# Kernel optimization log

Hardware: AMD Instinct MI355X
Metric: run time of the kernel (lower is better)

Reference implementation:

```python
import jax, jax.numpy as jnp
import numpy as np

STATE_LEN = 128
SEQ_LEN = 2048
NUM_ITERS = 2
DIM_IN = 1024
DIM_H = 64
BATCH = 2
T_TOTAL = SEQ_LEN + 2 * STATE_LEN  # 2304
NEG = -1e30  # large-negative causal mask (avoids -inf NaNs under autodiff)


def _ln(x, g, b):
    m = jnp.mean(x, axis=-1, keepdims=True)
    v = jnp.var(x, axis=-1, keepdims=True)
    return (x - m) / jnp.sqrt(v + 1e-5) * g + b


def setup_inputs() -> dict:
    key = jax.random.key(0)
    ks = jax.random.split(key, 16)

    def w(k, fi, fo):
        # torch nn.Linear-style fan-in scaled init (keeps logits O(1))
        return jax.random.normal(k, (fi, fo), jnp.float32) / np.sqrt(fi)

    return {
        "x": jax.random.normal(ks[0], (BATCH, T_TOTAL, DIM_IN), jnp.float32),
        "Wh": w(ks[1], DIM_IN, DIM_H),
        "Whs": w(ks[2], DIM_IN, DIM_H),
        "Whe": w(ks[3], DIM_IN, DIM_H),
        "Wk": w(ks[4], DIM_H, DIM_H),
        "Wq": w(ks[5], DIM_H, DIM_H),
        "Wv": w(ks[6], DIM_H, DIM_H),
        "Wks": w(ks[7], DIM_H, DIM_H),
        "Wqs": w(ks[8], DIM_H, DIM_H),
        "Wvs": w(ks[9], DIM_H, DIM_H),
        "Wke": w(ks[10], DIM_H, DIM_H),
        "Wqe": w(ks[11], DIM_H, DIM_H),
        "Wve": w(ks[12], DIM_H, DIM_H),
        "ln_g": jnp.ones((DIM_IN,), jnp.float32),
        "ln_b": jnp.zeros((DIM_IN,), jnp.float32),
        "ln_gs": jnp.ones((DIM_IN,), jnp.float32),
        "ln_bs": jnp.zeros((DIM_IN,), jnp.float32),
        "ln_ge": jnp.ones((DIM_IN,), jnp.float32),
        "ln_be": jnp.zeros((DIM_IN,), jnp.float32),
        "cope_emb": jax.random.normal(ks[13], (DIM_H, T_TOTAL), jnp.float32),
    }


def reference(x, Wh, Whs, Whe, Wk, Wq, Wv, Wks, Wqs, Wvs, Wke, Wqe, Wve,
              ln_g, ln_b, ln_gs, ln_bs, ln_ge, ln_be, cope_emb):
    S = STATE_LEN
    # extract_state: [state_start | seq | state_end] along token dim
    xs, xm, xe = x[:, :S], x[:, S:-S], x[:, -S:]
    xm = _ln(xm, ln_g, ln_b)
    xs = _ln(xs, ln_gs, ln_bs)
    xe = _ln(xe, ln_ge, ln_be)

    mem = xm @ Wh                 # (B, L, D)
    mem_s = xs @ Whs              # (B, S, D)
    mem_e = xe @ Whe              # (B, S, D)

    scale = 1.0 / np.sqrt(DIM_H)  # xformers default scale (beta=None)
    tril = jnp.tril(jnp.ones((T_TOTAL, T_TOTAL), bool))
    mask = jnp.where(tril, 0.0, NEG)  # log of lower-triangular ones

    mem_full = None
    for ix in range(NUM_ITERS):
        k = jnp.concatenate([mem_s @ Wks, mem @ Wk, mem_e @ Wke], axis=1)  # (B,T,D)
        q = jnp.concatenate([mem_s @ Wqs, mem @ Wq, mem_e @ Wqe], axis=1)
        v = jnp.concatenate([mem_s @ Wvs, mem @ Wv, mem_e @ Wve], axis=1)

        logits = jnp.einsum('btd,bsd->bts', q, k)  # unscaled, as in CoPE gates
        if ix == 0:
            # CoPE: sigmoid-gated reverse cumsum positions + interpolated embedding bias
            gates = jax.nn.sigmoid(logits)
            pos = jnp.flip(jnp.cumsum(jnp.flip(gates, -1), axis=-1), -1)
            pos = jnp.minimum(pos, float(T_TOTAL - 1))
            pos_floor = jnp.floor(pos)
            pos_ceil = jnp.ceil(pos)
            logits_int = jnp.einsum('btd,dn->btn', q, cope_emb)  # (B,T,T)
            lc = jnp.take_along_axis(logits_int, pos_ceil.astype(jnp.int32), axis=-1)
            lf = jnp.take_along_axis(logits_int, pos_floor.astype(jnp.int32), axis=-1)
            wfrac = pos - pos_floor
            bias = lc * wfrac + lf * (1.0 - wfrac)
            scores = logits * scale + mask + bias
        else:
            scores = logits * scale + mask

        attn = jax.nn.softmax(scores, axis=-1)
        mem_full = jnp.einsum('bts,bsd->btd', attn, v)  # (B,T,D)
        if ix < NUM_ITERS - 1:
            mem_s, mem, mem_e = mem_full[:, :S], mem_full[:, S:-S], mem_full[:, -S:]
    return mem_full
```

## Files before the change

### kernel.cpp

```cpp
#include <hip/hip_runtime.h>

#define T_TOT 2304
#define S_LEN 128
#define D_IN  1024
#define D_H   64
#define BATCH 2
#define NROW  (BATCH * T_TOT)
#define CH    (T_TOT / 256)
#define SCALE 0.125f
#define KCHUNKS 8
#define KCW   (D_IN / KCHUNKS)

typedef unsigned short u16;
typedef __attribute__((ext_vector_type(8))) short short8;
typedef __attribute__((ext_vector_type(4))) float f32x4;
typedef __attribute__((ext_vector_type(4))) unsigned short u16x4;

static __device__ __forceinline__ u16 f2bf(float f) {
    unsigned u = __float_as_uint(f);
    unsigned r = (u + 0x7fffu + ((u >> 16) & 1u)) >> 16;
    return (u16)r;
}
static __device__ __forceinline__ float bf2f(u16 s) {
    return __uint_as_float((unsigned)s << 16);
}

__global__ __launch_bounds__(256) void k_ln(
    const float* __restrict__ x,
    const float* __restrict__ ln_g,  const float* __restrict__ ln_b,
    const float* __restrict__ ln_gs, const float* __restrict__ ln_bs,
    const float* __restrict__ ln_ge, const float* __restrict__ ln_be,
    u16* __restrict__ xn_hi, u16* __restrict__ xn_lo)
{
    __shared__ float red1[256], red2[256];
    const int row = blockIdx.x;
    const int t = row % T_TOT;
    const int tid = threadIdx.x;

    const float *gg, *bb;
    if (t < S_LEN)               { gg = ln_gs; bb = ln_bs; }
    else if (t >= T_TOT - S_LEN) { gg = ln_ge; bb = ln_be; }
    else                         { gg = ln_g;  bb = ln_b;  }

    const float4 xv = *(const float4*)(x + (size_t)row * D_IN + 4 * tid);
    float s  = xv.x + xv.y + xv.z + xv.w;
    float s2 = xv.x * xv.x + xv.y * xv.y + xv.z * xv.z + xv.w * xv.w;
    red1[tid] = s; red2[tid] = s2; __syncthreads();
    for (int off = 128; off > 0; off >>= 1) {
        if (tid < off) { red1[tid] += red1[tid + off]; red2[tid] += red2[tid + off]; }
        __syncthreads();
    }
    const float mean = red1[0] * (1.f / D_IN);
    const float var  = red2[0] * (1.f / D_IN) - mean * mean;
    const float rstd = rsqrtf(var + 1e-5f);

    const float4 gv = *(const float4*)(gg + 4 * tid);
    const float4 bv = *(const float4*)(bb + 4 * tid);
    float o0 = (xv.x - mean) * rstd * gv.x + bv.x;
    float o1 = (xv.y - mean) * rstd * gv.y + bv.y;
    float o2 = (xv.z - mean) * rstd * gv.z + bv.z;
    float o3 = (xv.w - mean) * rstd * gv.w + bv.w;

    u16x4 hv, lv;
    hv[0] = f2bf(o0); lv[0] = f2bf(o0 - bf2f(hv[0]));
    hv[1] = f2bf(o1); lv[1] = f2bf(o1 - bf2f(hv[1]));
    hv[2] = f2bf(o2); lv[2] = f2bf(o2 - bf2f(hv[2]));
    hv[3] = f2bf(o3); lv[3] = f2bf(o3 - bf2f(hv[3]));
    *(u16x4*)(xn_hi + (size_t)row * D_IN + 4 * tid) = hv;
    *(u16x4*)(xn_lo + (size_t)row * D_IN + 4 * tid) = lv;
}

#define WPREP_N (3 * D_H * D_IN)
__global__ __launch_bounds__(256) void k_prep(
    const float* __restrict__ Wh, const float* __restrict__ Whs, const float* __restrict__ Whe,
    const float* __restrict__ cope,
    u16* __restrict__ wT_hi, u16* __restrict__ wT_lo,
    u16* __restrict__ cT_hi, u16* __restrict__ cT_lo)
{
    const int gid = blockIdx.x * 256 + threadIdx.x;
    if (gid < WPREP_N) {
        const int seg = gid >> 16;
        const int o = gid & 65535;
        const int j = o >> 10, k = o & 1023;
        const float* W = seg == 0 ? Wh : (seg == 1 ? Whs : Whe);
        const float f = W[k * D_H + j];
        const u16 hi = f2bf(f);
        wT_hi[gid] = hi;
        wT_lo[gid] = f2bf(f - bf2f(hi));
    } else {
        const int idx = gid - WPREP_N;
        if (idx < T_TOT * D_H) {
            const int n = idx >> 6, d = idx & 63;
            const float f = cope[(size_t)d * T_TOT + n];
            const u16 hi = f2bf(f);
            cT_hi[idx] = hi;
            cT_lo[idx] = f2bf(f - bf2f(hi));
        }
    }
}

__global__ __launch_bounds__(256) void k_hgemm(
    const u16* __restrict__ xn_hi, const u16* __restrict__ xn_lo,
    const u16* __restrict__ wT_hi, const u16* __restrict__ wT_lo,
    float* __restrict__ h_part)
{
    const int tile = blockIdx.x;
    const int kc   = blockIdx.y;
    const int k0   = kc * KCW;
    const int tt = tile % 36;
    const int seg = tt < 2 ? 1 : (tt >= 34 ? 2 : 0);

    __shared__ u16 Bh[64 * KCW];
    __shared__ u16 Bl[64 * KCW];

    const int tid = threadIdx.x;
    {
        const int r = tid >> 2;
        const int c0 = (tid & 3) * 32;
        const u16* sh = wT_hi + ((size_t)seg * D_H + r) * D_IN + k0 + c0;
        const u16* sl = wT_lo + ((size_t)seg * D_H + r) * D_IN + k0 + c0;
        const int sw = (r & 7) << 3;
        #pragma unroll
        for (int u = 0; u < 4; ++u) {
            const int col = c0 + 8 * u;
            *(short8*)&Bh[r * KCW + (col ^ sw)] = *(const short8*)(sh + 8 * u);
            *(short8*)&Bl[r * KCW + (col ^ sw)] = *(const short8*)(sl + 8 * u);
        }
    }
    __syncthreads();

    const int w = tid >> 6;
    const int lane = tid & 63;
    const int l15 = lane & 15, lg4 = lane >> 4;
    const int row0 = tile * 64 + w * 16;

    const size_t abase = (size_t)(row0 + l15) * D_IN + k0 + 8 * lg4;
    f32x4 acc[4] = {};

    #pragma unroll
    for (int kk = 0; kk < KCW / 32; ++kk) {
        short8 ah = *(const short8*)(xn_hi + abase + kk * 32);
        short8 al = *(const short8*)(xn_lo + abase + kk * 32);
        #pragma unroll
        for (int j = 0; j < 4; ++j) {
            const int brow = j * 16 + l15;
            const int col = (kk * 32 + 8 * lg4) ^ ((brow & 7) << 3);
            short8 bh = *(const short8*)&Bh[brow * KCW + col];
            short8 bl = *(const short8*)&Bl[brow * KCW + col];
            acc[j] = __builtin_amdgcn_mfma_f32_16x16x32_bf16(al, bh, acc[j], 0, 0, 0);
            acc[j] = __builtin_amdgcn_mfma_f32_16x16x32_bf16(ah, bl, acc[j], 0, 0, 0);
            acc[j] = __builtin_amdgcn_mfma_f32_16x16x32_bf16(ah, bh, acc[j], 0, 0, 0);
        }
    }
    float* hp = h_part + (size_t)kc * ((size_t)NROW * D_H);
    #pragma unroll
    for (int j = 0; j < 4; ++j)
        #pragma unroll
        for (int r = 0; r < 4; ++r)
            hp[(size_t)(row0 + 4 * lg4 + r) * D_H + j * 16 + l15] = acc[j][r];
}

__global__ __launch_bounds__(256) void k_hred(
    const float* __restrict__ h_part, float* __restrict__ h)
{
    const size_t idx = (size_t)blockIdx.x * 256 + threadIdx.x;
    const size_t N = (size_t)NROW * D_H;
    float s = 0.f;
    #pragma unroll
    for (int kc = 0; kc < KCHUNKS; ++kc) s += h_part[kc * N + idx];
    h[idx] = s;
}

template <bool SPLIT>
__global__ __launch_bounds__(192) void k_qkv(
    const float* __restrict__ hin,
    const float* __restrict__ Wk,  const float* __restrict__ Wq,  const float* __restrict__ Wv,
    const float* __restrict__ Wks, const float* __restrict__ Wqs, const float* __restrict__ Wvs,
    const float* __restrict__ Wke, const float* __restrict__ Wqe, const float* __restrict__ Wve,
    u16* __restrict__ q_hi, u16* __restrict__ q_lo,
    u16* __restrict__ k_hi, u16* __restrict__ k_lo,
    u16* __restrict__ vT)
{
    __shared__ float hr[D_H];
    const int bid = blockIdx.x;
    const int b = bid / T_TOT, t = bid % T_TOT;
    const int tid = threadIdx.x;

    const float* hrow = hin + ((size_t)b * T_TOT + t) * D_H;
    if (tid < D_H) hr[tid] = hrow[tid];
    __syncthreads();

    const int which = tid >> 6, j = tid & 63;
    const float* W;
    if (t < S_LEN)               W = which == 0 ? Wks : (which == 1 ? Wqs : Wvs);
    else if (t >= T_TOT - S_LEN) W = which == 0 ? Wke : (which == 1 ? Wqe : Wve);
    else                         W = which == 0 ? Wk  : (which == 1 ? Wq  : Wv);

    float acc = 0.f;
    #pragma unroll
    for (int d = 0; d < D_H; ++d) acc += hr[d] * W[d * D_H + j];

    const size_t idx = ((size_t)b * T_TOT + t) * D_H + j;
    u16 hi = f2bf(acc);
    if (which == 0) {
        k_hi[idx] = hi;
        if (SPLIT) k_lo[idx] = f2bf(acc - bf2f(hi));
    } else if (which == 1) {
        q_hi[idx] = hi;
        if (SPLIT) q_lo[idx] = f2bf(acc - bf2f(hi));
    } else {
        vT[((size_t)b * D_H + j) * T_TOT + t] = hi;
    }
}

__global__ __launch_bounds__(256) void k_score2(
    const u16* __restrict__ a_hi, const u16* __restrict__ a_lo,
    const u16* __restrict__ k_hi, const u16* __restrict__ k_lo,
    const u16* __restrict__ c_hi, const u16* __restrict__ c_lo,
    float* __restrict__ logits, float* __restrict__ lint)
{
    const int b  = blockIdx.z;
    const int s0 = blockIdx.x * 128;
    const int t0 = blockIdx.y * 64 + (threadIdx.x >> 6) * 16;
    const int lane = threadIdx.x & 63;
    const int l15 = lane & 15, lg4 = lane >> 4;

    const size_t a_off = ((size_t)(b * T_TOT + t0 + l15)) * D_H + 8 * lg4;
    const short8 ah0 = *(const short8*)(a_hi + a_off);
    const short8 ah1 = *(const short8*)(a_hi + a_off + 32);
    const short8 al0 = *(const short8*)(a_lo + a_off);
    const short8 al1 = *(const short8*)(a_lo + a_off + 32);

    const size_t orow_off = ((size_t)(b * T_TOT + t0 + 4 * lg4)) * T_TOT + s0 + l15;

    const u16* bh = k_hi + (size_t)b * (T_TOT * D_H);
    const u16* bl = k_lo + (size_t)b * (T_TOT * D_H);
    float* o = logits + orow_off;
    #pragma unroll
    for (int pass = 0; pass < 2; ++pass) {
        #pragma unroll
        for (int ni = 0; ni < 8; ++ni) {
            const size_t b_off = ((size_t)(s0 + ni * 16 + l15)) * D_H + 8 * lg4;
            short8 bh0 = *(const short8*)(bh + b_off);
            short8 bh1 = *(const short8*)(bh + b_off + 32);
            short8 bl0 = *(const short8*)(bl + b_off);
            short8 bl1 = *(const short8*)(bl + b_off + 32);
            f32x4 acc = {0.f, 0.f, 0.f, 0.f};
            acc = __builtin_amdgcn_mfma_f32_16x16x32_bf16(al0, bh0, acc, 0, 0, 0);
            acc = __builtin_amdgcn_mfma_f32_16x16x32_bf16(al1, bh1, acc, 0, 0, 0);
            acc = __builtin_amdgcn_mfma_f32_16x16x32_bf16(ah0, bl0, acc, 0, 0, 0);
            acc = __builtin_amdgcn_mfma_f32_16x16x32_bf16(ah1, bl1, acc, 0, 0, 0);
            acc = __builtin_amdgcn_mfma_f32_16x16x32_bf16(ah0, bh0, acc, 0, 0, 0);
            acc = __builtin_amdgcn_mfma_f32_16x16x32_bf16(ah1, bh1, acc, 0, 0, 0);
            #pragma unroll
            for (int r = 0; r < 4; ++r)
                o[(size_t)r * T_TOT + ni * 16] = acc[r];
        }
        bh = c_hi; bl = c_lo;
        o = lint + orow_off;
    }
}

__global__ __launch_bounds__(256) void k_score(
    const u16* __restrict__ a_hi, const u16* __restrict__ b_hi,
    float* __restrict__ out)
{
    const int b  = blockIdx.z;
    const int s0 = blockIdx.x * 128;
    if (s0 > blockIdx.y * 64 + 63) return;
    const int t0 = blockIdx.y * 64 + (threadIdx.x >> 6) * 16;
    const int lane = threadIdx.x & 63;
    const int l15 = lane & 15, lg4 = lane >> 4;

    const size_t a_off = ((size_t)(b * T_TOT + t0 + l15)) * D_H + 8 * lg4;
    short8 ah0 = *(const short8*)(a_hi + a_off);
    short8 ah1 = *(const short8*)(a_hi + a_off + 32);

    const u16* bh = b_hi + (size_t)b * (T_TOT * D_H);
    float* orow = out + ((size_t)(b * T_TOT + t0 + 4 * lg4)) * T_TOT + s0 + l15;

    #pragma unroll
    for (int ni = 0; ni < 8; ++ni) {
        const size_t b_off = ((size_t)(s0 + ni * 16 + l15)) * D_H + 8 * lg4;
        short8 bh0 = *(const short8*)(bh + b_off);
        short8 bh1 = *(const short8*)(bh + b_off + 32);
        f32x4 acc = {0.f, 0.f, 0.f, 0.f};
        acc = __builtin_amdgcn_mfma_f32_16x16x32_bf16(ah0, bh0, acc, 0, 0, 0);
        acc = __builtin_amdgcn_mfma_f32_16x16x32_bf16(ah1, bh1, acc, 0, 0, 0);
        #pragma unroll
        for (int r = 0; r < 4; ++r)
            orow[(size_t)r * T_TOT + ni * 16] = acc[r];
    }
}

__global__ __launch_bounds__(256) void k_pv(
    const float* __restrict__ pbuf, const u16* __restrict__ vT,
    float* __restrict__ out)
{
    const int b  = blockIdx.z;
    const int t0 = blockIdx.x * 16;
    const int j0 = (threadIdx.x >> 6) * 16;
    const int lane = threadIdx.x & 63;
    const int l15 = lane & 15, lg4 = lane >> 4;

    const u16* pb = (const u16*)pbuf
        + ((size_t)(b * T_TOT + t0 + l15)) * (2 * (size_t)T_TOT) + 8 * lg4;
    const u16* vb = vT + ((size_t)(b * D_H + j0 + l15)) * T_TOT + 8 * lg4;

    f32x4 a0 = {}, a1 = {}, a2 = {}, a3 = {};
    const int smax = t0 + 16;
    int sc = 0;
    for (; sc + 128 <= smax; sc += 128) {
        short8 p0 = *(const short8*)(pb + sc);
        short8 v0 = *(const short8*)(vb + sc);
        short8 p1 = *(const short8*)(pb + sc + 32);
        short8 v1 = *(const short8*)(vb + sc + 32);
        short8 p2 = *(const short8*)(pb + sc + 64);
        short8 v2 = *(const short8*)(vb + sc + 64);
        short8 p3 = *(const short8*)(pb + sc + 96);
        short8 v3 = *(const short8*)(vb + sc + 96);
        a0 = __builtin_amdgcn_mfma_f32_16x16x32_bf16(p0, v0, a0, 0, 0, 0);
        a1 = __builtin_amdgcn_mfma_f32_16x16x32_bf16(p1, v1, a1, 0, 0, 0);
        a2 = __builtin_amdgcn_mfma_f32_16x16x32_bf16(p2, v2, a2, 0, 0, 0);
        a3 = __builtin_amdgcn_mfma_f32_16x16x32_bf16(p3, v3, a3, 0, 0, 0);
    }
    for (; sc < smax; sc += 32) {
        short8 p0 = *(const short8*)(pb + sc);
        short8 v0 = *(const short8*)(vb + sc);
        a0 = __builtin_amdgcn_mfma_f32_16x16x32_bf16(p0, v0, a0, 0, 0, 0);
    }
    f32x4 acc = (a0 + a1) + (a2 + a3);
    float* obase = out + ((size_t)(b * T_TOT + t0 + 4 * lg4)) * D_H + j0 + l15;
    #pragma unroll
    for (int r = 0; r < 4; ++r) obase[(size_t)r * D_H] = acc[r];
}

template <bool COPE>
__global__ __launch_bounds__(256) void k_erow(
    const float* __restrict__ logits,
    const float* __restrict__ lint,
    float* __restrict__ pbase)
{
    __shared__ float lg[T_TOT];
    __shared__ float extra[COPE ? 2 * T_TOT : 2];
    __shared__ float wtot[4], wmax[4], wsum[4];

    const int row = blockIdx.x;
    const int t = row % T_TOT;
    const int tid = threadIdx.x;
    const int lane = tid & 63, wid = tid >> 6;
    const float* lrow = logits + (size_t)row * T_TOT;

    if (COPE) {
        for (int r = 0; r < CH; ++r) { int s = tid + 256 * r; lg[s] = lrow[s]; }
    } else {
        for (int r = 0; r < CH; ++r) { int s = tid + 256 * r; if (s <= t) lg[s] = lrow[s]; }
    }
    __syncthreads();

    if (COPE) {
        const int base = tid * CH;
        float gv[CH];
        float lsum = 0.f;
        #pragma unroll
        for (int u = 0; u < CH; ++u) {
            float g = 1.f / (1.f + expf(-lg[base + u]));
            gv[u] = g;
            lsum += g;
        }
        float cs = lsum;
        #pragma unroll
        for (int off = 1; off < 64; off <<= 1) {
            float n = __shfl_up(cs, off);
            if (lane >= off) cs += n;
        }
        if (lane == 63) wtot[wid] = cs;
        __syncthreads();
        float pre = 0.f, tot = 0.f;
        #pragma unroll
        for (int w = 0; w < 4; ++w) {
            float vv = wtot[w];
            tot += vv;
            if (w < wid) pre += vv;
        }
        float run = pre + cs - lsum;
        #pragma unroll
        for (int u = 0; u < CH; ++u) {
            float p = fminf(tot - run, (float)(T_TOT - 1));
            extra[base + u] = p;
            run += gv[u];
        }
        const float* lintrow = lint + (size_t)row * T_TOT;
        for (int r = 0; r < CH; ++r) { int s = tid + 256 * r; extra[T_TOT + s] = lintrow[s]; }
        __syncthreads();
    }

    float scv[CH];
    float mx = -3.4e38f;
    #pragma unroll
    for (int r = 0; r < CH; ++r) {
        int sidx = tid + 256 * r;
        float sc = -3.4e38f;
        if (sidx <= t) {
            sc = lg[sidx] * SCALE;
            if (COPE) {
                float p = extra[sidx];
                float pf = floorf(p);
                int fi = (int)pf;
                int ci = (int)ceilf(p);
                float w = p - pf;
                sc += extra[T_TOT + ci] * w + extra[T_TOT + fi] * (1.f - w);
            }
            mx = fmaxf(mx, sc);
        }
        scv[r] = sc;
    }
    #pragma unroll
    for (int off = 32; off > 0; off >>= 1) mx = fmaxf(mx, __shfl_xor(mx, off));
    if (lane == 0) wmax[wid] = mx;
    __syncthreads();
    mx = fmaxf(fmaxf(wmax[0], wmax[1]), fmaxf(wmax[2], wmax[3]));

    float pvv[CH];
    float psum = 0.f;
    #pragma unroll
    for (int r = 0; r < CH; ++r) {
        int sidx = tid + 256 * r;
        float pv = 0.f;
        if (sidx <= t) { pv = expf(scv[r] - mx); psum += pv; }
        pvv[r] = pv;
    }
    #pragma unroll
    for (int off = 32; off > 0; off >>= 1) psum += __shfl_xor(psum, off);
    if (lane == 0) wsum[wid] = psum;
    __syncthreads();
    const float inv = 1.f / (wsum[0] + wsum[1] + wsum[2] + wsum[3]);

    u16* prow = (u16*)(pbase + (size_t)row * T_TOT);
    #pragma unroll
    for (int r = 0; r < CH; ++r) {
        int sidx = tid + 256 * r;
        prow[sidx] = f2bf(pvv[r] * inv);
    }
}

extern "C" void kernel_launch(void* const* d_in, const int* in_sizes, int n_in,
                              void* d_out, int out_size, void* d_ws, size_t ws_size,
                              hipStream_t stream) {
    const float* x    = (const float*)d_in[0];
    const float* Wh   = (const float*)d_in[1];
    const float* Whs  = (const float*)d_in[2];
    const float* Whe  = (const float*)d_in[3];
    const float* Wk   = (const float*)d_in[4];
    const float* Wq   = (const float*)d_in[5];
    const float* Wv   = (const float*)d_in[6];
    const float* Wks  = (const float*)d_in[7];
    const float* Wqs  = (const float*)d_in[8];
    const float* Wvs  = (const float*)d_in[9];
    const float* Wke  = (const float*)d_in[10];
    const float* Wqe  = (const float*)d_in[11];
    const float* Wve  = (const float*)d_in[12];
    const float* ln_g  = (const float*)d_in[13];
    const float* ln_b  = (const float*)d_in[14];
    const float* ln_gs = (const float*)d_in[15];
    const float* ln_bs = (const float*)d_in[16];
    const float* ln_ge = (const float*)d_in[17];
    const float* ln_be = (const float*)d_in[18];
    const float* cope  = (const float*)d_in[19];

    float* out = (float*)d_out;

    const size_t N = (size_t)NROW * D_H;
    char* W = (char*)d_ws;
    u16* xn_hi  = (u16*)W;    W += (size_t)NROW * D_IN * 2;
    u16* xn_lo  = (u16*)W;    W += (size_t)NROW * D_IN * 2;
    u16* wT_hi  = (u16*)W;    W += (size_t)3 * D_H * D_IN * 2;
    u16* wT_lo  = (u16*)W;    W += (size_t)3 * D_H * D_IN * 2;
    float* h    = (float*)W;  W += N * 4;
    u16* q_hi   = (u16*)W;    W += N * 2;
    u16* q_lo   = (u16*)W;    W += N * 2;
    u16* k_hi   = (u16*)W;    W += N * 2;
    u16* k_lo   = (u16*)W;    W += N * 2;
    u16* vT     = (u16*)W;    W += N * 2;
    u16* cT_hi  = (u16*)W;    W += (size_t)T_TOT * D_H * 2;
    u16* cT_lo  = (u16*)W;    W += (size_t)T_TOT * D_H * 2;
    float* logits = (float*)W; W += (size_t)BATCH * T_TOT * T_TOT * 4;
    float* lint   = (float*)W; W += (size_t)BATCH * T_TOT * T_TOT * 4;
    float* mem1   = (float*)W;

    float* h_part = lint;

    const dim3 sg(T_TOT / 128, T_TOT / 64, BATCH);

    k_ln<<<NROW, 256, 0, stream>>>(x, ln_g, ln_b, ln_gs, ln_bs, ln_ge, ln_be,
                                   xn_hi, xn_lo);
    k_prep<<<(WPREP_N + T_TOT * D_H + 255) / 256, 256, 0, stream>>>(
        Wh, Whs, Whe, cope, wT_hi, wT_lo, cT_hi, cT_lo);
    k_hgemm<<<dim3(NROW / 64, KCHUNKS), 256, 0, stream>>>(xn_hi, xn_lo, wT_hi, wT_lo, h_part);
    k_hred<<<(int)(N / 256), 256, 0, stream>>>(h_part, h);

    k_qkv<true><<<NROW, 192, 0, stream>>>(h, Wk, Wq, Wv, Wks, Wqs, Wvs, Wke, Wqe, Wve,
                                          q_hi, q_lo, k_hi, k_lo, vT);
    k_score2<<<sg, 256, 0, stream>>>(q_hi, q_lo, k_hi, k_lo, cT_hi, cT_lo, logits, lint);
    k_erow<true><<<NROW, 256, 0, stream>>>(logits, lint, lint);
    k_pv<<<dim3(T_TOT / 16, 1, BATCH), 256, 0, stream>>>(lint, vT, mem1);

    k_qkv<false><<<NROW, 192, 0, stream>>>(mem1, Wk, Wq, Wv, Wks, Wqs, Wvs, Wke, Wqe, Wve,
                                           q_hi, q_lo, k_hi, k_lo, vT);
    k_score<<<sg, 256, 0, stream>>>(q_hi, k_hi, logits);
    k_erow<false><<<NROW, 256, 0, stream>>>(logits, nullptr, lint);
    k_pv<<<dim3(T_TOT / 16, 1, BATCH), 256, 0, stream>>>(lint, vT, out);
}
```

Before: 189.4 us.

## Fuse second attention iteration into split-K flash attention and split PV

Replaces the second iteration's score, softmax-row and PV kernels with a flash-attention kernel that computes scores, online softmax and PV per 16-row tile across key chunks, followed by a merge kernel. This removes the full T×T logits write and read for the second pass. The first-pass PV is also split over key chunks with a reduction kernel to balance the causal triangle, and the first score kernel uses 64-wide column tiles for more blocks. It adds extra partial buffers and merge launches, and uses bf16 P with online rescaling.

```diff
diff --git a/kernel.cpp b/kernel.cpp
--- a/kernel.cpp
+++ b/kernel.cpp
@@ -10,6 +10,10 @@
 #define SCALE 0.125f
 #define KCHUNKS 8
 #define KCW   (D_IN / KCHUNKS)
+#define TB    16
+#define FCH   288
+#define NSC   8
+#define NTBLK (T_TOT / TB)
 
 typedef unsigned short u16;
 typedef __attribute__((ext_vector_type(8))) short short8;
@@ -220,8 +224,9 @@
     float* __restrict__ logits, float* __restrict__ lint)
 {
     const int b  = blockIdx.z;
-    const int s0 = blockIdx.x * 128;
-    const int t0 = blockIdx.y * 64 + (threadIdx.x >> 6) * 16;
+    const int s0 = blockIdx.x * 64;
+    const int wid = threadIdx.x >> 6;
+    const int t0 = blockIdx.y * 64 + wid * 16;
     const int lane = threadIdx.x & 63;
     const int l15 = lane & 15, lg4 = lane >> 4;
 
@@ -236,10 +241,11 @@
     const u16* bh = k_hi + (size_t)b * (T_TOT * D_H);
     const u16* bl = k_lo + (size_t)b * (T_TOT * D_H);
     float* o = logits + orow_off;
+
     #pragma unroll
     for (int pass = 0; pass < 2; ++pass) {
         #pragma unroll
-        for (int ni = 0; ni < 8; ++ni) {
+        for (int ni = 0; ni < 4; ++ni) {
             const size_t b_off = ((size_t)(s0 + ni * 16 + l15)) * D_H + 8 * lg4;
             short8 bh0 = *(const short8*)(bh + b_off);
             short8 bh1 = *(const short8*)(bh + b_off + 32);
@@ -261,88 +267,13 @@
     }
 }
 
-__global__ __launch_bounds__(256) void k_score(
-    const u16* __restrict__ a_hi, const u16* __restrict__ b_hi,
-    float* __restrict__ out)
-{
-    const int b  = blockIdx.z;
-    const int s0 = blockIdx.x * 128;
-    if (s0 > blockIdx.y * 64 + 63) return;
-    const int t0 = blockIdx.y * 64 + (threadIdx.x >> 6) * 16;
-    const int lane = threadIdx.x & 63;
-    const int l15 = lane & 15, lg4 = lane >> 4;
-
-    const size_t a_off = ((size_t)(b * T_TOT + t0 + l15)) * D_H + 8 * lg4;
-    short8 ah0 = *(const short8*)(a_hi + a_off);
-    short8 ah1 = *(const short8*)(a_hi + a_off + 32);
-
-    const u16* bh = b_hi + (size_t)b * (T_TOT * D_H);
-    float* orow = out + ((size_t)(b * T_TOT + t0 + 4 * lg4)) * T_TOT + s0 + l15;
-
-    #pragma unroll
-    for (int ni = 0; ni < 8; ++ni) {
-        const size_t b_off = ((size_t)(s0 + ni * 16 + l15)) * D_H + 8 * lg4;
-        short8 bh0 = *(const short8*)(bh + b_off);
-        short8 bh1 = *(const short8*)(bh + b_off + 32);
-        f32x4 acc = {0.f, 0.f, 0.f, 0.f};
-        acc = __builtin_amdgcn_mfma_f32_16x16x32_bf16(ah0, bh0, acc, 0, 0, 0);
-        acc = __builtin_amdgcn_mfma_f32_16x16x32_bf16(ah1, bh1, acc, 0, 0, 0);
-        #pragma unroll
-        for (int r = 0; r < 4; ++r)
-            orow[(size_t)r * T_TOT + ni * 16] = acc[r];
-    }
-}
-
-__global__ __launch_bounds__(256) void k_pv(
-    const float* __restrict__ pbuf, const u16* __restrict__ vT,
-    float* __restrict__ out)
-{
-    const int b  = blockIdx.z;
-    const int t0 = blockIdx.x * 16;
-    const int j0 = (threadIdx.x >> 6) * 16;
-    const int lane = threadIdx.x & 63;
-    const int l15 = lane & 15, lg4 = lane >> 4;
-
-    const u16* pb = (const u16*)pbuf
-        + ((size_t)(b * T_TOT + t0 + l15)) * (2 * (size_t)T_TOT) + 8 * lg4;
-    const u16* vb = vT + ((size_t)(b * D_H + j0 + l15)) * T_TOT + 8 * lg4;
-
-    f32x4 a0 = {}, a1 = {}, a2 = {}, a3 = {};
-    const int smax = t0 + 16;
-    int sc = 0;
-    for (; sc + 128 <= smax; sc += 128) {
-        short8 p0 = *(const short8*)(pb + sc);
-        short8 v0 = *(const short8*)(vb + sc);
-        short8 p1 = *(const short8*)(pb + sc + 32);
-        short8 v1 = *(const short8*)(vb + sc + 32);
-        short8 p2 = *(const short8*)(pb + sc + 64);
-        short8 v2 = *(const short8*)(vb + sc + 64);
-        short8 p3 = *(const short8*)(pb + sc + 96);
-        short8 v3 = *(const short8*)(vb + sc + 96);
-        a0 = __builtin_amdgcn_mfma_f32_16x16x32_bf16(p0, v0, a0, 0, 0, 0);
-        a1 = __builtin_amdgcn_mfma_f32_16x16x32_bf16(p1, v1, a1, 0, 0, 0);
-        a2 = __builtin_amdgcn_mfma_f32_16x16x32_bf16(p2, v2, a2, 0, 0, 0);
-        a3 = __builtin_amdgcn_mfma_f32_16x16x32_bf16(p3, v3, a3, 0, 0, 0);
-    }
-    for (; sc < smax; sc += 32) {
-        short8 p0 = *(const short8*)(pb + sc);
-        short8 v0 = *(const short8*)(vb + sc);
-        a0 = __builtin_amdgcn_mfma_f32_16x16x32_bf16(p0, v0, a0, 0, 0, 0);
-    }
-    f32x4 acc = (a0 + a1) + (a2 + a3);
-    float* obase = out + ((size_t)(b * T_TOT + t0 + 4 * lg4)) * D_H + j0 + l15;
-    #pragma unroll
-    for (int r = 0; r < 4; ++r) obase[(size_t)r * D_H] = acc[r];
-}
-
-template <bool COPE>
 __global__ __launch_bounds__(256) void k_erow(
     const float* __restrict__ logits,
     const float* __restrict__ lint,
     float* __restrict__ pbase)
 {
     __shared__ float lg[T_TOT];
-    __shared__ float extra[COPE ? 2 * T_TOT : 2];
+    __shared__ float extra[2 * T_TOT];
     __shared__ float wtot[4], wmax[4], wsum[4];
 
     const int row = blockIdx.x;
@@ -351,14 +282,10 @@
     const int lane = tid & 63, wid = tid >> 6;
     const float* lrow = logits + (size_t)row * T_TOT;
 
-    if (COPE) {
-        for (int r = 0; r < CH; ++r) { int s = tid + 256 * r; lg[s] = lrow[s]; }
-    } else {
-        for (int r = 0; r < CH; ++r) { int s = tid + 256 * r; if (s <= t) lg[s] = lrow[s]; }
-    }
+    for (int r = 0; r < CH; ++r) { int s = tid + 256 * r; lg[s] = lrow[s]; }
     __syncthreads();
 
-    if (COPE) {
+    {
         const int base = tid * CH;
         float gv[CH];
         float lsum = 0.f;
@@ -403,14 +330,12 @@
         float sc = -3.4e38f;
         if (sidx <= t) {
             sc = lg[sidx] * SCALE;
-            if (COPE) {
-                float p = extra[sidx];
-                float pf = floorf(p);
-                int fi = (int)pf;
-                int ci = (int)ceilf(p);
-                float w = p - pf;
-                sc += extra[T_TOT + ci] * w + extra[T_TOT + fi] * (1.f - w);
-            }
+            float p = extra[sidx];
+            float pf = floorf(p);
+            int fi = (int)pf;
+            int ci = (int)ceilf(p);
+            float w = p - pf;
+            sc += extra[T_TOT + ci] * w + extra[T_TOT + fi] * (1.f - w);
             mx = fmaxf(mx, sc);
         }
         scv[r] = sc;
@@ -442,6 +367,205 @@
         int sidx = tid + 256 * r;
         prow[sidx] = f2bf(pvv[r] * inv);
     }
+}
+
+__global__ __launch_bounds__(256) void k_pv(
+    const float* __restrict__ pbuf, const u16* __restrict__ vT,
+    float* __restrict__ opart)
+{
+    const int b  = blockIdx.z;
+    const int scn = blockIdx.y;
+    const int bx = blockIdx.x;
+    const int t0 = bx * 16;
+    const int sstart = scn * FCH;
+    const int send = min(sstart + FCH, t0 + 16);
+    if (sstart >= send) return;
+
+    const int j0 = (threadIdx.x >> 6) * 16;
+    const int lane = threadIdx.x & 63;
+    const int l15 = lane & 15, lg4 = lane >> 4;
+
+    const u16* pb = (const u16*)pbuf
+        + ((size_t)(b * T_TOT + t0 + l15)) * (2 * (size_t)T_TOT) + 8 * lg4;
+    const u16* vb = vT + ((size_t)(b * D_H + j0 + l15)) * T_TOT + 8 * lg4;
+
+    f32x4 a0 = {}, a1 = {}, a2 = {}, a3 = {};
+    int s = sstart;
+    for (; s + 128 <= send; s += 128) {
+        short8 p0 = *(const short8*)(pb + s);
+        short8 v0 = *(const short8*)(vb + s);
+        short8 p1 = *(const short8*)(pb + s + 32);
+        short8 v1 = *(const short8*)(vb + s + 32);
+        short8 p2 = *(const short8*)(pb + s + 64);
+        short8 v2 = *(const short8*)(vb + s + 64);
+        short8 p3 = *(const short8*)(pb + s + 96);
+        short8 v3 = *(const short8*)(vb + s + 96);
+        a0 = __builtin_amdgcn_mfma_f32_16x16x32_bf16(p0, v0, a0, 0, 0, 0);
+        a1 = __builtin_amdgcn_mfma_f32_16x16x32_bf16(p1, v1, a1, 0, 0, 0);
+        a2 = __builtin_amdgcn_mfma_f32_16x16x32_bf16(p2, v2, a2, 0, 0, 0);
+        a3 = __builtin_amdgcn_mfma_f32_16x16x32_bf16(p3, v3, a3, 0, 0, 0);
+    }
+    for (; s < send; s += 32) {
+        short8 p0 = *(const short8*)(pb + s);
+        short8 v0 = *(const short8*)(vb + s);
+        a0 = __builtin_amdgcn_mfma_f32_16x16x32_bf16(p0, v0, a0, 0, 0, 0);
+    }
+    f32x4 acc = (a0 + a1) + (a2 + a3);
+    float* ob = opart + (((size_t)(b * NTBLK + bx)) * NSC + scn) * (TB * D_H)
+              + (size_t)(4 * lg4) * D_H + j0 + l15;
+    #pragma unroll
+    for (int r = 0; r < 4; ++r) ob[(size_t)r * D_H] = acc[r];
+}
+
+__global__ __launch_bounds__(256) void k_pvmerge(
+    const float* __restrict__ opart, float* __restrict__ outp)
+{
+    const int bid = blockIdx.x;
+    const int b = bid / NTBLK, bx = bid % NTBLK;
+    const int t0 = bx * 16, t_max = t0 + 15;
+    const int tid = threadIdx.x;
+    const int tl = tid >> 4, j4 = (tid & 15) * 4;
+
+    float4 acc = {0.f, 0.f, 0.f, 0.f};
+    for (int scn = 0; scn < NSC; ++scn) {
+        if (scn * FCH <= t_max) {
+            const float4 v = *(const float4*)&opart[
+                (((size_t)(b * NTBLK + bx)) * NSC + scn) * (TB * D_H) + tl * D_H + j4];
+            acc.x += v.x; acc.y += v.y; acc.z += v.z; acc.w += v.w;
+        }
+    }
+    *(float4*)&outp[((size_t)(b * T_TOT + t0 + tl)) * D_H + j4] = acc;
+}
+
+__global__ __launch_bounds__(256) void k_fattn1s(
+    const u16* __restrict__ q_hi, const u16* __restrict__ k_hi,
+    const u16* __restrict__ vT,
+    float* __restrict__ fM, float* __restrict__ fD, float* __restrict__ fO)
+{
+    __shared__ u16 pstage[4][TB][32];
+
+    const int b   = blockIdx.z;
+    const int scn = blockIdx.y;
+    const int bx  = blockIdx.x;
+    const int t0 = bx * TB;
+    const int t_max = t0 + TB - 1;
+    if (scn * FCH > t_max) return;
+
+    const int tid = threadIdx.x;
+    const int wid = tid >> 6;
+    const int lane = tid & 63;
+    const int l15 = lane & 15, lg4 = lane >> 4;
+
+    const size_t a_off = ((size_t)(b * T_TOT + t0 + l15)) * D_H + 8 * lg4;
+    const short8 ah0 = *(const short8*)(q_hi + a_off);
+    const short8 ah1 = *(const short8*)(q_hi + a_off + 32);
+    const u16* kh = k_hi + (size_t)b * (T_TOT * D_H);
+
+    const int w_lo  = scn * FCH + wid * (FCH / 4);
+    const int w_end = min(w_lo + FCH / 4, t_max + 1);
+
+    float m[4]   = {-3.0e38f, -3.0e38f, -3.0e38f, -3.0e38f};
+    float den[4] = {0.f, 0.f, 0.f, 0.f};
+    f32x4 oacc[4] = {};
+
+    for (int s32 = w_lo; s32 < w_end; s32 += 32) {
+        f32x4 acc0 = {0.f, 0.f, 0.f, 0.f};
+        f32x4 acc1 = {0.f, 0.f, 0.f, 0.f};
+        const bool ir1 = (s32 + 16) < w_end;
+        {
+            const size_t b_off = ((size_t)(s32 + l15)) * D_H + 8 * lg4;
+            short8 b0 = *(const short8*)(kh + b_off);
+            short8 b1 = *(const short8*)(kh + b_off + 32);
+            acc0 = __builtin_amdgcn_mfma_f32_16x16x32_bf16(ah0, b0, acc0, 0, 0, 0);
+            acc0 = __builtin_amdgcn_mfma_f32_16x16x32_bf16(ah1, b1, acc0, 0, 0, 0);
+        }
+        if (ir1) {
+            const size_t b_off = ((size_t)(s32 + 16 + l15)) * D_H + 8 * lg4;
+            short8 b0 = *(const short8*)(kh + b_off);
+            short8 b1 = *(const short8*)(kh + b_off + 32);
+            acc1 = __builtin_amdgcn_mfma_f32_16x16x32_bf16(ah0, b0, acc1, 0, 0, 0);
+            acc1 = __builtin_amdgcn_mfma_f32_16x16x32_bf16(ah1, b1, acc1, 0, 0, 0);
+        }
+        #pragma unroll
+        for (int r = 0; r < 4; ++r) {
+            const int tl = 4 * lg4 + r;
+            const int c0 = s32 + l15, c1 = s32 + 16 + l15;
+            const bool v0 = (c0 < w_end) && (c0 <= t0 + tl);
+            const bool v1 = ir1 && (c1 < w_end) && (c1 <= t0 + tl);
+            const float sc0 = acc0[r] * SCALE;
+            const float sc1 = acc1[r] * SCALE;
+            float tmx = fmaxf(v0 ? sc0 : -3.0e38f, v1 ? sc1 : -3.0e38f);
+            tmx = fmaxf(tmx, __shfl_xor(tmx, 1));
+            tmx = fmaxf(tmx, __shfl_xor(tmx, 2));
+            tmx = fmaxf(tmx, __shfl_xor(tmx, 4));
+            tmx = fmaxf(tmx, __shfl_xor(tmx, 8));
+            const float mn = fmaxf(m[r], tmx);
+            const float scl = __expf(m[r] - mn);
+            m[r] = mn;
+            const float p0 = v0 ? __expf(sc0 - mn) : 0.f;
+            const float p1 = v1 ? __expf(sc1 - mn) : 0.f;
+            float ps = p0 + p1;
+            ps += __shfl_xor(ps, 1); ps += __shfl_xor(ps, 2);
+            ps += __shfl_xor(ps, 4); ps += __shfl_xor(ps, 8);
+            den[r] = den[r] * scl + ps;
+            #pragma unroll
+            for (int j = 0; j < 4; ++j) oacc[j][r] *= scl;
+            pstage[wid][tl][l15] = f2bf(p0);
+            pstage[wid][tl][16 + l15] = f2bf(p1);
+        }
+        const short8 pa = *(const short8*)&pstage[wid][l15][8 * lg4];
+        #pragma unroll
+        for (int j = 0; j < 4; ++j) {
+            const size_t v_off = ((size_t)(b * D_H + j * 16 + l15)) * T_TOT + s32 + 8 * lg4;
+            short8 bv = *(const short8*)(vT + v_off);
+            oacc[j] = __builtin_amdgcn_mfma_f32_16x16x32_bf16(pa, bv, oacc[j], 0, 0, 0);
+        }
+    }
+
+    const size_t pidx = ((size_t)(b * NTBLK + bx)) * (NSC * 4) + scn * 4 + wid;
+    if (l15 == 0) {
+        #pragma unroll
+        for (int r = 0; r < 4; ++r) {
+            fM[pidx * TB + 4 * lg4 + r] = m[r];
+            fD[pidx * TB + 4 * lg4 + r] = den[r];
+        }
+    }
+    #pragma unroll
+    for (int j = 0; j < 4; ++j)
+        #pragma unroll
+        for (int r = 0; r < 4; ++r)
+            fO[pidx * (TB * D_H) + (size_t)(4 * lg4 + r) * D_H + j * 16 + l15] = oacc[j][r];
+}
+
+__global__ __launch_bounds__(256) void k_fmerge(
+    const float* __restrict__ fM, const float* __restrict__ fD,
+    const float* __restrict__ fO, float* __restrict__ outp)
+{
+    const int bid = blockIdx.x;
+    const int b = bid / NTBLK, bx = bid % NTBLK;
+    const int t0 = bx * 16, t_max = t0 + 15;
+    const int tid = threadIdx.x;
+    const int tl = tid >> 4, j4 = (tid & 15) * 4;
+    const size_t pb = (size_t)bid * (NSC * 4);
+
+    float M = -3.0e38f;
+    #pragma unroll
+    for (int c = 0; c < NSC * 4; ++c)
+        if ((c >> 2) * FCH <= t_max) M = fmaxf(M, fM[(pb + c) * TB + tl]);
+
+    float D = 0.f;
+    float4 O = {0.f, 0.f, 0.f, 0.f};
+    for (int c = 0; c < NSC * 4; ++c) {
+        if ((c >> 2) * FCH <= t_max) {
+            const float w = __expf(fM[(pb + c) * TB + tl] - M);
+            D += w * fD[(pb + c) * TB + tl];
+            const float4 ov = *(const float4*)&fO[(pb + c) * (TB * D_H) + tl * D_H + j4];
+            O.x += w * ov.x; O.y += w * ov.y; O.z += w * ov.z; O.w += w * ov.w;
+        }
+    }
+    const float inv = 1.f / D;
+    float4 res; res.x = O.x * inv; res.y = O.y * inv; res.z = O.z * inv; res.w = O.w * inv;
+    *(float4*)&outp[((size_t)(b * T_TOT + t0 + tl)) * D_H + j4] = res;
 }
 
 extern "C" void kernel_launch(void* const* d_in, const int* in_sizes, int n_in,
@@ -486,11 +610,13 @@
     u16* cT_lo  = (u16*)W;    W += (size_t)T_TOT * D_H * 2;
     float* logits = (float*)W; W += (size_t)BATCH * T_TOT * T_TOT * 4;
     float* lint   = (float*)W; W += (size_t)BATCH * T_TOT * T_TOT * 4;
-    float* mem1   = (float*)W;
+    float* mem1   = (float*)W; W += N * 4;
+    float* opart  = (float*)W; W += (size_t)BATCH * NTBLK * NSC * TB * D_H * 4;
+    float* fM     = (float*)W; W += (size_t)BATCH * NTBLK * NSC * 4 * TB * 4;
+    float* fD     = (float*)W; W += (size_t)BATCH * NTBLK * NSC * 4 * TB * 4;
+    float* fO     = (float*)W; W += (size_t)BATCH * NTBLK * NSC * 4 * TB * D_H * 4;
 
     float* h_part = lint;
-
-    const dim3 sg(T_TOT / 128, T_TOT / 64, BATCH);
 
     k_ln<<<NROW, 256, 0, stream>>>(x, ln_g, ln_b, ln_gs, ln_bs, ln_ge, ln_be,
                                    xn_hi, xn_lo);
@@ -501,13 +627,14 @@
 
     k_qkv<true><<<NROW, 192, 0, stream>>>(h, Wk, Wq, Wv, Wks, Wqs, Wvs, Wke, Wqe, Wve,
                                           q_hi, q_lo, k_hi, k_lo, vT);
-    k_score2<<<sg, 256, 0, stream>>>(q_hi, q_lo, k_hi, k_lo, cT_hi, cT_lo, logits, lint);
-    k_erow<true><<<NROW, 256, 0, stream>>>(logits, lint, lint);
-    k_pv<<<dim3(T_TOT / 16, 1, BATCH), 256, 0, stream>>>(lint, vT, mem1);
+    k_score2<<<dim3(T_TOT / 64, T_TOT / 64, BATCH), 256, 0, stream>>>(
+        q_hi, q_lo, k_hi, k_lo, cT_hi, cT_lo, logits, lint);
+    k_erow<<<NROW, 256, 0, stream>>>(logits, lint, lint);
+    k_pv<<<dim3(NTBLK, NSC, BATCH), 256, 0, stream>>>(lint, vT, opart);
+    k_pvmerge<<<BATCH * NTBLK, 256, 0, stream>>>(opart, mem1);
 
     k_qkv<false><<<NROW, 192, 0, stream>>>(mem1, Wk, Wq, Wv, Wks, Wqs, Wvs, Wke, Wqe, Wve,
                                            q_hi, q_lo, k_hi, k_lo, vT);
-    k_score<<<sg, 256, 0, stream>>>(q_hi, k_hi, logits);
-    k_erow<false><<<NROW, 256, 0, stream>>>(logits, nullptr, lint);
-    k_pv<<<dim3(T_TOT / 16, 1, BATCH), 256, 0, stream>>>(lint, vT, out);
-}
+    k_fattn1s<<<dim3(NTBLK, NSC, BATCH), 256, 0, stream>>>(q_hi, k_hi, vT, fM, fD, fO);
+    k_fmerge<<<BATCH * NTBLK, 256, 0, stream>>>(fM, fD, fO, out);
+}
```

Measured after the change: 182.1 us. 1.04x faster.
